# Kernel tuning notes

Measured on AMD Instinct MI355X. Metric: run time of the kernel, lower is better.

## Reference

```python
import jax, jax.numpy as jnp
import numpy as np

EPS = 2.0 ** (-20)  # FP16_tiny
Q_DIM = 256
M_DIM = 256
NUM_HEAD = 8
KEY_DIM = Q_DIM // NUM_HEAD   # 32 per head
VAL_DIM = M_DIM // NUM_HEAD   # 32 per head
OUT_DIM = 256
B, R, S = 1, 256, 1024


def setup_inputs() -> dict:
    key = jax.random.key(0)
    ks = jax.random.split(key, 12)
    q_data = jax.random.normal(ks[0], (B, R, S, Q_DIM), dtype=jnp.float32)
    m_data = jax.random.normal(ks[1], (B, R, S, M_DIM), dtype=jnp.float32)
    q_mask = (jax.random.uniform(ks[2], (B, R, S, 1)) > 0.1).astype(jnp.float32)
    bias = jax.random.normal(ks[3], (B, R, 1, S), dtype=jnp.float32) * 0.1
    # weights stored as [in, out] (torch Linear applies x @ W.T; equivalent math)
    gl = lambda k, i, o: jax.random.normal(k, (i, o), dtype=jnp.float32) * (6.0 / (i + o)) ** 0.5
    Wq = gl(ks[4], Q_DIM, NUM_HEAD * KEY_DIM)
    Wk = gl(ks[5], M_DIM, KEY_DIM)
    Wv = gl(ks[6], M_DIM, VAL_DIM)
    # linear_o has 'final' init (zeros) in the original; use small random for a useful baseline
    Wo = jax.random.normal(ks[7], (NUM_HEAD * VAL_DIM, OUT_DIM), dtype=jnp.float32) * 0.02
    bo = jnp.zeros((OUT_DIM,), dtype=jnp.float32)
    # linear_g: 'gating' init is W=0, b=1; use small random W for non-degenerate test
    Wg = jax.random.normal(ks[8], (Q_DIM, NUM_HEAD * VAL_DIM), dtype=jnp.float32) * 0.02
    bg = jnp.ones((NUM_HEAD * VAL_DIM,), dtype=jnp.float32)
    return {"q_data": q_data, "m_data": m_data, "q_mask": q_mask, "bias": bias,
            "Wq": Wq, "Wk": Wk, "Wv": Wv, "Wo": Wo, "bo": bo, "Wg": Wg, "bg": bg}


def reference(q_data, m_data, q_mask, bias, Wq, Wk, Wv, Wo, bo, Wg, bg):
    key_scalar = KEY_DIM ** (-0.5)
    # masked mean pool over the sequence (N_seq) axis -> [B,R,q_dim]
    q_avg = jnp.sum(q_data * q_mask, axis=-2) / (jnp.sum(q_mask, axis=-2) + EPS)
    q = (q_avg @ Wq) * key_scalar                       # [B,R,H*kd]
    q = q.reshape(q.shape[:-1] + (NUM_HEAD, KEY_DIM))    # [B,R,H,kd]
    k = m_data @ Wk                                      # [B,R,S,kd]
    v = m_data @ Wv                                      # [B,R,S,vd]
    logits = jnp.einsum('brhd,brsd->brhs', q, k) + bias  # [B,R,H,S]
    weight = jax.nn.softmax(logits, axis=-1)
    weighted_avg = jnp.einsum('brhs,brsd->brhd', weight, v)  # [B,R,H,vd]
    # gating
    g = jax.nn.sigmoid(q_data @ Wg + bg)                 # [B,R,S,H*vd]
    g = g.reshape(g.shape[:-1] + (NUM_HEAD, VAL_DIM))     # [B,R,S,H,vd]
    gated = weighted_avg[:, :, None] * g                  # [B,R,S,H,vd]
    gated = gated.reshape(gated.shape[:-2] + (NUM_HEAD * VAL_DIM,))
    out = gated @ Wo + bo                                 # [B,R,S,out_dim]
    return out
```

## Files before the change

kernel.cpp:

```cpp
#include <hip/hip_runtime.h>
#include <stdint.h>

typedef __bf16 bf16x8 __attribute__((ext_vector_type(8)));
typedef float f32x4 __attribute__((ext_vector_type(4)));
typedef unsigned short ushort8 __attribute__((ext_vector_type(8)));
typedef unsigned short u16x4 __attribute__((ext_vector_type(4)));

#define S_DIM 1024
#define R_DIM 256
#define DMODEL 256
#define EPSV 9.5367431640625e-07f
#define ASTRIDE 264
#define OSTRIDE 72

__device__ __forceinline__ unsigned short f2bf(float f) {
  uint32_t u = __float_as_uint(f);
  u += 0x7fffu + ((u >> 16) & 1u);
  return (unsigned short)(u >> 16);
}
__device__ __forceinline__ float bf2f(unsigned short s) {
  return __uint_as_float(((uint32_t)s) << 16);
}
__device__ __forceinline__ bf16x8 ldfrag(const unsigned short* p) {
  return __builtin_bit_cast(bf16x8, *(const ushort8*)p);
}
__device__ __forceinline__ bf16x8 pack8(float4 a, float4 b) {
  ushort8 u;
  u[0] = f2bf(a.x); u[1] = f2bf(a.y); u[2] = f2bf(a.z); u[3] = f2bf(a.w);
  u[4] = f2bf(b.x); u[5] = f2bf(b.y); u[6] = f2bf(b.z); u[7] = f2bf(b.w);
  return __builtin_bit_cast(bf16x8, u);
}

__global__ __launch_bounds__(256) void pack_all_kernel(const float* __restrict__ Wk,
                                                       const float* __restrict__ Wv,
                                                       const float* __restrict__ Wg,
                                                       const float* __restrict__ Wo,
                                                       unsigned short* __restrict__ wkv,
                                                       unsigned short* __restrict__ wg_p,
                                                       unsigned short* __restrict__ wo_p) {
  int bid = blockIdx.x;
  int tid = threadIdx.x;
  if (bid < 64) {
    int idx = bid * 256 + tid;
    int j = idx & 7, lane = (idx >> 3) & 63, t = idx >> 9;
    int ct = t & 3, kstep = t >> 2;
    int k = kstep * 32 + ((lane >> 4) << 3) + j;
    int col = ct * 16 + (lane & 15);
    float w = (col < 32) ? Wk[k * 32 + col] : Wv[k * 32 + (col - 32)];
    wkv[idx] = f2bf(w);
  } else {
    const float* W = (bid < 320) ? Wg : Wo;
    unsigned short* out = (bid < 320) ? wg_p : wo_p;
    int idx = ((bid < 320) ? (bid - 64) : (bid - 320)) * 256 + tid;
    int j = idx & 7, lane = (idx >> 3) & 63, t = idx >> 9;
    int ct = t & 15, kstep = t >> 4;
    int k = kstep * 32 + ((lane >> 4) << 3) + j;
    int col = ct * 16 + (lane & 15);
    out[idx] = f2bf(W[k * 256 + col]);
  }
}

template <int USE_ECHO>
__global__ __launch_bounds__(512, 4) void pool_kernel(const float* __restrict__ q_data,
                                                      const float* __restrict__ q_mask,
                                                      float* __restrict__ psum,
                                                      float* __restrict__ pmask,
                                                      unsigned short* __restrict__ qb16) {
  __shared__ float mlds[256];
  __shared__ float wred[4];
  __shared__ f32x4 red[8 * 64];
  int bid = blockIdx.x;
  int tid = threadIdx.x;
  int r = bid >> 2, c = bid & 3;
  int s0 = c * 256;
  if (tid < 256) {
    float m = q_mask[r * S_DIM + s0 + tid];
    mlds[tid] = m;
    float ms = m;
    for (int off = 32; off; off >>= 1) ms += __shfl_down(ms, off);
    if ((tid & 63) == 0) wred[tid >> 6] = ms;
  }
  __syncthreads();
  if (tid == 0) pmask[r * 4 + c] = wred[0] + wred[1] + wred[2] + wred[3];
  int wv = tid >> 6, ln = tid & 63;
  size_t rowbase = (size_t)(r * S_DIM + s0);
  const float* bp = q_data + (rowbase + wv) * DMODEL + ln * 4;
  unsigned short* ebp = USE_ECHO ? (qb16 + (rowbase + wv) * DMODEL + ln * 4) : nullptr;
  f32x4 acc4 = {};
  #pragma unroll 8
  for (int it = 0; it < 32; it++) {
    float4 v = *(const float4*)(bp + (size_t)it * 8 * DMODEL);
    float mm = mlds[it * 8 + wv];
    acc4[0] += v.x * mm; acc4[1] += v.y * mm;
    acc4[2] += v.z * mm; acc4[3] += v.w * mm;
    if (USE_ECHO) {
      u16x4 e;
      e[0] = f2bf(v.x); e[1] = f2bf(v.y); e[2] = f2bf(v.z); e[3] = f2bf(v.w);
      *(u16x4*)(ebp + (size_t)it * 8 * DMODEL) = e;
    }
  }
  red[wv * 64 + ln] = acc4;
  __syncthreads();
  if (tid < 256) {
    int c4 = tid >> 2, cm = tid & 3;
    float sum = 0.f;
    #pragma unroll
    for (int k = 0; k < 8; k++) sum += red[k * 64 + c4][cm];
    psum[(r * 4 + c) * 256 + tid] = sum;
  }
}

__global__ __launch_bounds__(256, 8) void kv_kernel(const float* __restrict__ m_data,
                                                    const unsigned short* __restrict__ wkv,
                                                    unsigned short* __restrict__ kb,
                                                    unsigned short* __restrict__ vb_t) {
  __shared__ __align__(16) unsigned short As[32 * ASTRIDE];
  int bid = blockIdx.x;
  int tid = threadIdx.x;
  int wave = tid >> 6, lane = tid & 63;
  int g = lane >> 4, lr = lane & 15;
  int row0 = bid * 32;
  #pragma unroll
  for (int i = 0; i < 4; i++) {
    int c = i * 256 + tid;
    int ra = c >> 5, cc = c & 31;
    const float4* p = (const float4*)&m_data[(size_t)(row0 + ra) * DMODEL + cc * 8];
    *(ushort8*)&As[ra * ASTRIDE + cc * 8] = __builtin_bit_cast(ushort8, pack8(p[0], p[1]));
  }
  __syncthreads();
  int rt = wave >> 1, cp = (wave & 1) * 2;
  f32x4 acc[2] = {};
  #pragma unroll
  for (int ks = 0; ks < 8; ks++) {
    bf16x8 af = ldfrag(&As[(rt * 16 + lr) * ASTRIDE + ks * 32 + g * 8]);
    #pragma unroll
    for (int cc2 = 0; cc2 < 2; cc2++) {
      bf16x8 bf = ldfrag(&wkv[((ks * 4 + cp + cc2) << 9) + lane * 8]);
      acc[cc2] = __builtin_amdgcn_mfma_f32_16x16x32_bf16(af, bf, acc[cc2], 0, 0, 0);
    }
  }
  __syncthreads();
  unsigned short* O = As;
  #pragma unroll
  for (int cc2 = 0; cc2 < 2; cc2++) {
    #pragma unroll
    for (int rg = 0; rg < 4; rg++) {
      O[(rt * 16 + g * 4 + rg) * OSTRIDE + (cp + cc2) * 16 + lr] = f2bf(acc[cc2][rg]);
    }
  }
  __syncthreads();
  {
    int rowl = tid >> 3, c4 = (tid & 7) * 4;
    u16x4 v = *(const u16x4*)&O[rowl * OSTRIDE + c4];
    *(u16x4*)&kb[(size_t)(row0 + rowl) * 32 + c4] = v;
  }
  if (tid < 128) {
    int d = tid >> 2, s8 = (tid & 3) * 8;
    ushort8 v;
    #pragma unroll
    for (int j = 0; j < 8; j++) v[j] = O[(s8 + j) * OSTRIDE + 32 + d];
    int ra = row0 >> 10, sl0 = row0 & 1023;
    *(ushort8*)&vb_t[((size_t)(ra * 32) + d) * S_DIM + sl0 + s8] = v;
  }
}

__global__ __launch_bounds__(256) void attn2_kernel(const unsigned short* __restrict__ kb,
                                                    const unsigned short* __restrict__ vb_t,
                                                    const float* __restrict__ psum,
                                                    const float* __restrict__ pmask,
                                                    const float* __restrict__ Wq,
                                                    const float* __restrict__ bias,
                                                    float* __restrict__ wavg) {
  int r = blockIdx.x, tid = threadIdx.x;
  int w = tid >> 6, lane = tid & 63, g = lane >> 4, lr = lane & 15;
  __shared__ float qa[256];
  __shared__ float qsp[8 * 33];
  __shared__ float lgp[8 * 1028];
  __shared__ float paccL[8 * 64 * 4];
  __shared__ float denom[8];
  float s4 = psum[(r * 4 + 0) * 256 + tid] + psum[(r * 4 + 1) * 256 + tid] +
             psum[(r * 4 + 2) * 256 + tid] + psum[(r * 4 + 3) * 256 + tid];
  float msum = pmask[r * 4] + pmask[r * 4 + 1] + pmask[r * 4 + 2] + pmask[r * 4 + 3];
  qa[tid] = s4 / (msum + EPSV);
  __syncthreads();
  float qacc = 0.f;
  #pragma unroll 8
  for (int d = 0; d < 256; d++) qacc += qa[d] * Wq[d * 256 + tid];
  qsp[(tid >> 5) * 33 + (tid & 31)] = qacc * 0.17677669529663687f;
  __syncthreads();
  ushort8 uq;
  #pragma unroll
  for (int j = 0; j < 8; j++)
    uq[j] = (lr < 8) ? f2bf(qsp[lr * 33 + g * 8 + j]) : (unsigned short)0;
  bf16x8 qf = __builtin_bit_cast(bf16x8, uq);
  for (int i = 0; i < 16; i++) {
    int rt = w * 16 + i;
    bf16x8 af = ldfrag(&kb[((size_t)r * S_DIM + rt * 16 + lr) * 32 + g * 8]);
    f32x4 d4 = {};
    d4 = __builtin_amdgcn_mfma_f32_16x16x32_bf16(af, qf, d4, 0, 0, 0);
    if (lr < 8) {
      #pragma unroll
      for (int rg = 0; rg < 4; rg++) {
        int sv = rt * 16 + g * 4 + rg;
        lgp[lr * 1028 + sv] = d4[rg] + bias[r * S_DIM + sv];
      }
    }
  }
  __syncthreads();
  for (int hh = 0; hh < 2; hh++) {
    int h = w * 2 + hh;
    float mx = -1e30f;
    #pragma unroll
    for (int i = 0; i < 16; i++) mx = fmaxf(mx, lgp[h * 1028 + lane + i * 64]);
    for (int off = 32; off; off >>= 1) mx = fmaxf(mx, __shfl_xor(mx, off));
    float sum = 0.f;
    #pragma unroll
    for (int i = 0; i < 16; i++) {
      float e = __expf(lgp[h * 1028 + lane + i * 64] - mx);
      lgp[h * 1028 + lane + i * 64] = e;
      sum += e;
    }
    for (int off = 32; off; off >>= 1) sum += __shfl_xor(sum, off);
    if (lane == 0) denom[h] = sum;
  }
  __syncthreads();
  f32x4 pv[2] = {};
  for (int kk = 0; kk < 8; kk++) {
    int ks = w * 8 + kk;
    bf16x8 pa;
    if (lr < 8) {
      const float4* pp = (const float4*)&lgp[lr * 1028 + ks * 32 + g * 8];
      pa = pack8(*(const float4*)&pp[0], *(const float4*)&pp[1]);
    } else {
      pa = __builtin_bit_cast(bf16x8, (ushort8)(unsigned short)0);
    }
    #pragma unroll
    for (int ct = 0; ct < 2; ct++) {
      bf16x8 vf = ldfrag(&vb_t[((size_t)(r * 32) + ct * 16 + lr) * S_DIM + ks * 32 + g * 8]);
      pv[ct] = __builtin_amdgcn_mfma_f32_16x16x32_bf16(pa, vf, pv[ct], 0, 0, 0);
    }
  }
  *(f32x4*)&paccL[((w * 2 + 0) * 64 + lane) * 4] = pv[0];
  *(f32x4*)&paccL[((w * 2 + 1) * 64 + lane) * 4] = pv[1];
  __syncthreads();
  {
    int h = tid >> 5, d = tid & 31;
    int ct = d >> 4, l2 = (h >> 2) * 16 + (d & 15), rg = h & 3;
    float sum = 0.f;
    #pragma unroll
    for (int w4 = 0; w4 < 4; w4++) sum += paccL[((w4 * 2 + ct) * 64 + l2) * 4 + rg];
    wavg[r * 256 + tid] = __fdividef(sum, denom[h]);
  }
}

template <int USE_BF16>
__global__ __launch_bounds__(512, 4) void gate3_kernel(const float* __restrict__ q_data,
                                                       const unsigned short* __restrict__ qb16,
                                                       const unsigned short* __restrict__ wg,
                                                       const unsigned short* __restrict__ wo,
                                                       const float* __restrict__ bgv,
                                                       const float* __restrict__ bov,
                                                       const float* __restrict__ wavg,
                                                       float* __restrict__ outp) {
  __shared__ unsigned short AsG[64 * ASTRIDE];
  __shared__ float wavs[256];
  __shared__ float bgs[256];
  __shared__ float bos[256];
  int bid = blockIdx.x;
  int r = bid >> 4, sc = bid & 15;
  int tid = threadIdx.x;
  int wave = tid >> 6, lane = tid & 63, g = lane >> 4, lr = lane & 15;
  int row0g = r * S_DIM + sc * 64;
  if (tid < 256) {
    wavs[tid] = wavg[r * 256 + tid];
    bgs[tid] = bgv[tid];
    bos[tid] = bov[tid];
  }
  #pragma unroll
  for (int i = 0; i < 4; i++) {
    int c = i * 512 + tid;
    int ra = c >> 5, cc = c & 31;
    ushort8 v;
    if (USE_BF16) {
      v = *(const ushort8*)&qb16[(size_t)(row0g + ra) * DMODEL + cc * 8];
    } else {
      const float4* p = (const float4*)&q_data[(size_t)(row0g + ra) * DMODEL + cc * 8];
      v = __builtin_bit_cast(ushort8, pack8(p[0], p[1]));
    }
    *(ushort8*)&AsG[ra * ASTRIDE + cc * 8] = v;
  }
  __syncthreads();
  f32x4 acc[4][2] = {};
  for (int ks = 0; ks < 8; ks++) {
    bf16x8 b0 = ldfrag(&wg[((ks * 16 + 2 * wave) << 9) + lane * 8]);
    bf16x8 b1 = ldfrag(&wg[((ks * 16 + 2 * wave + 1) << 9) + lane * 8]);
    bf16x8 af[4];
    #pragma unroll
    for (int rt = 0; rt < 4; rt++)
      af[rt] = ldfrag(&AsG[(rt * 16 + lr) * ASTRIDE + ks * 32 + g * 8]);
    #pragma unroll
    for (int rt = 0; rt < 4; rt++) {
      acc[rt][0] = __builtin_amdgcn_mfma_f32_16x16x32_bf16(af[rt], b0, acc[rt][0], 0, 0, 0);
      acc[rt][1] = __builtin_amdgcn_mfma_f32_16x16x32_bf16(af[rt], b1, acc[rt][1], 0, 0, 0);
    }
  }
  __syncthreads();
  #pragma unroll
  for (int rt = 0; rt < 4; rt++) {
    #pragma unroll
    for (int c0 = 0; c0 < 2; c0++) {
      int col = (wave * 2 + c0) * 16 + lr;
      float wv = wavs[col];
      float bgc = bgs[col];
      #pragma unroll
      for (int rg = 0; rg < 4; rg++) {
        int row = rt * 16 + g * 4 + rg;
        float x = acc[rt][c0][rg] + bgc;
        float sg = __fdividef(1.0f, 1.0f + __expf(-x));
        AsG[row * ASTRIDE + col] = f2bf(sg * wv);
      }
    }
  }
  __syncthreads();
  f32x4 acc2[4][2] = {};
  for (int ks = 0; ks < 8; ks++) {
    bf16x8 b0 = ldfrag(&wo[((ks * 16 + 2 * wave) << 9) + lane * 8]);
    bf16x8 b1 = ldfrag(&wo[((ks * 16 + 2 * wave + 1) << 9) + lane * 8]);
    bf16x8 af[4];
    #pragma unroll
    for (int rt = 0; rt < 4; rt++)
      af[rt] = ldfrag(&AsG[(rt * 16 + lr) * ASTRIDE + ks * 32 + g * 8]);
    #pragma unroll
    for (int rt = 0; rt < 4; rt++) {
      acc2[rt][0] = __builtin_amdgcn_mfma_f32_16x16x32_bf16(af[rt], b0, acc2[rt][0], 0, 0, 0);
      acc2[rt][1] = __builtin_amdgcn_mfma_f32_16x16x32_bf16(af[rt], b1, acc2[rt][1], 0, 0, 0);
    }
  }
  #pragma unroll
  for (int rt = 0; rt < 4; rt++) {
    #pragma unroll
    for (int c0 = 0; c0 < 2; c0++) {
      int col = (wave * 2 + c0) * 16 + lr;
      float boc = bos[col];
      #pragma unroll
      for (int rg = 0; rg < 4; rg++) {
        int row = rt * 16 + g * 4 + rg;
        outp[(size_t)(row0g + row) * DMODEL + col] = acc2[rt][c0][rg] + boc;
      }
    }
  }
}

extern "C" void kernel_launch(void* const* d_in, const int* in_sizes, int n_in,
                              void* d_out, int out_size, void* d_ws, size_t ws_size,
                              hipStream_t stream) {
  const float* q_data = (const float*)d_in[0];
  const float* m_data = (const float*)d_in[1];
  const float* q_mask = (const float*)d_in[2];
  const float* bias   = (const float*)d_in[3];
  const float* Wq     = (const float*)d_in[4];
  const float* Wk     = (const float*)d_in[5];
  const float* Wv     = (const float*)d_in[6];
  const float* Wo     = (const float*)d_in[7];
  const float* bo     = (const float*)d_in[8];
  const float* Wg     = (const float*)d_in[9];
  const float* bg     = (const float*)d_in[10];
  float* outp = (float*)d_out;

  char* ws = (char*)d_ws;
  unsigned short* kb      = (unsigned short*)(ws + 0);
  unsigned short* vb_t    = (unsigned short*)(ws + 16777216);
  unsigned short* wkv     = (unsigned short*)(ws + 33554432);
  unsigned short* wg_pack = (unsigned short*)(ws + 33587200);
  unsigned short* wo_pack = (unsigned short*)(ws + 33718272);
  float* psum  = (float*)(ws + 33849344);
  float* pmask = (float*)(ws + 34897920);
  float* wavg  = (float*)(ws + 35164160);
  const size_t QB16_OFF = 35651584;
  const size_t QB16_BYTES = (size_t)R_DIM * S_DIM * DMODEL * 2;
  bool use_echo = ws_size >= QB16_OFF + QB16_BYTES;
  unsigned short* qb16 = use_echo ? (unsigned short*)(ws + QB16_OFF) : nullptr;

  pack_all_kernel<<<576, 256, 0, stream>>>(Wk, Wv, Wg, Wo, wkv, wg_pack, wo_pack);
  kv_kernel<<<8192, 256, 0, stream>>>(m_data, wkv, kb, vb_t);
  if (use_echo)
    pool_kernel<1><<<1024, 512, 0, stream>>>(q_data, q_mask, psum, pmask, qb16);
  else
    pool_kernel<0><<<1024, 512, 0, stream>>>(q_data, q_mask, psum, pmask, nullptr);
  attn2_kernel<<<256, 256, 0, stream>>>(kb, vb_t, psum, pmask, Wq, bias, wavg);
  if (use_echo)
    gate3_kernel<1><<<4096, 512, 0, stream>>>(q_data, qb16, wg_pack, wo_pack, bg, bo, wavg, outp);
  else
    gate3_kernel<0><<<4096, 512, 0, stream>>>(q_data, nullptr, wg_pack, wo_pack, bg, bo, wavg, outp);
}
```

Baseline: 304.6 us.

## Use direct global-to-LDS loads in kv kernel and XCD-aware block remapping

The kv projection kernel now stages fp32 m_data rows straight into LDS through global_load_lds with an XOR swizzle. Conversion to bf16 moves to the fragment read, and the tile shrinks to 16 rows per block, which doubles the grid. The pool, kv and gate kernels also remap block IDs so consecutive work lands on the same XCD, aiming for better L2 locality across the chiplets. The trade-offs are twice the LDS footprint per row (fp32 instead of bf16), more blocks, and conversion work repeated inside the MFMA loop.

```diff
diff --git a/kernel.cpp b/kernel.cpp
--- a/kernel.cpp
+++ b/kernel.cpp
@@ -69,7 +69,8 @@
   __shared__ float mlds[256];
   __shared__ float wred[4];
   __shared__ f32x4 red[8 * 64];
-  int bid = blockIdx.x;
+  int bid0 = blockIdx.x;
+  int bid = (bid0 & 7) * 128 + (bid0 >> 3);
   int tid = threadIdx.x;
   int r = bid >> 2, c = bid & 3;
   int s0 = c * 256;
@@ -114,48 +115,45 @@
                                                     const unsigned short* __restrict__ wkv,
                                                     unsigned short* __restrict__ kb,
                                                     unsigned short* __restrict__ vb_t) {
-  __shared__ __align__(16) unsigned short As[32 * ASTRIDE];
-  int bid = blockIdx.x;
+  __shared__ __align__(16) float Af[16 * 256];
+  int bid0 = blockIdx.x;
+  int bid = (bid0 & 7) * 2048 + (bid0 >> 3);
   int tid = threadIdx.x;
   int wave = tid >> 6, lane = tid & 63;
   int g = lane >> 4, lr = lane & 15;
-  int row0 = bid * 32;
+  int row0 = bid * 16;
   #pragma unroll
   for (int i = 0; i < 4; i++) {
-    int c = i * 256 + tid;
-    int ra = c >> 5, cc = c & 31;
-    const float4* p = (const float4*)&m_data[(size_t)(row0 + ra) * DMODEL + cc * 8];
-    *(ushort8*)&As[ra * ASTRIDE + cc * 8] = __builtin_bit_cast(ushort8, pack8(p[0], p[1]));
-  }
-  __syncthreads();
-  int rt = wave >> 1, cp = (wave & 1) * 2;
-  f32x4 acc[2] = {};
+    int C = wave * 4 + i;
+    const char* gsrc = (const char*)(m_data + (size_t)(row0 + C) * DMODEL)
+                     + ((lane * 16) ^ ((C & 7) << 5));
+    __builtin_amdgcn_global_load_lds(
+        (const __attribute__((address_space(1))) void*)gsrc,
+        (__attribute__((address_space(3))) void*)(&Af[C * 256]), 16, 0, 0);
+  }
+  __syncthreads();
+  f32x4 acc = {};
   #pragma unroll
   for (int ks = 0; ks < 8; ks++) {
-    bf16x8 af = ldfrag(&As[(rt * 16 + lr) * ASTRIDE + ks * 32 + g * 8]);
-    #pragma unroll
-    for (int cc2 = 0; cc2 < 2; cc2++) {
-      bf16x8 bf = ldfrag(&wkv[((ks * 4 + cp + cc2) << 9) + lane * 8]);
-      acc[cc2] = __builtin_amdgcn_mfma_f32_16x16x32_bf16(af, bf, acc[cc2], 0, 0, 0);
-    }
-  }
-  __syncthreads();
-  unsigned short* O = As;
-  #pragma unroll
-  for (int cc2 = 0; cc2 < 2; cc2++) {
-    #pragma unroll
-    for (int rg = 0; rg < 4; rg++) {
-      O[(rt * 16 + g * 4 + rg) * OSTRIDE + (cp + cc2) * 16 + lr] = f2bf(acc[cc2][rg]);
-    }
-  }
-  __syncthreads();
-  {
+    int boff = (ks * 128 + g * 32) ^ ((lr & 7) << 5);
+    const float4* fp = (const float4*)((const char*)Af + lr * 1024 + boff);
+    bf16x8 af = pack8(fp[0], fp[1]);
+    bf16x8 bf = ldfrag(&wkv[((ks * 4 + wave) << 9) + lane * 8]);
+    acc = __builtin_amdgcn_mfma_f32_16x16x32_bf16(af, bf, acc, 0, 0, 0);
+  }
+  __syncthreads();
+  unsigned short* O = (unsigned short*)Af;
+  #pragma unroll
+  for (int rg = 0; rg < 4; rg++)
+    O[(g * 4 + rg) * OSTRIDE + wave * 16 + lr] = f2bf(acc[rg]);
+  __syncthreads();
+  if (tid < 128) {
     int rowl = tid >> 3, c4 = (tid & 7) * 4;
     u16x4 v = *(const u16x4*)&O[rowl * OSTRIDE + c4];
     *(u16x4*)&kb[(size_t)(row0 + rowl) * 32 + c4] = v;
-  }
-  if (tid < 128) {
-    int d = tid >> 2, s8 = (tid & 3) * 8;
+  } else if (tid < 192) {
+    int t = tid - 128;
+    int d = t >> 1, s8 = (t & 1) * 8;
     ushort8 v;
     #pragma unroll
     for (int j = 0; j < 8; j++) v[j] = O[(s8 + j) * OSTRIDE + 32 + d];
@@ -266,7 +264,8 @@
   __shared__ float wavs[256];
   __shared__ float bgs[256];
   __shared__ float bos[256];
-  int bid = blockIdx.x;
+  int bid0 = blockIdx.x;
+  int bid = (bid0 & 7) * 512 + (bid0 >> 3);
   int r = bid >> 4, sc = bid & 15;
   int tid = threadIdx.x;
   int wave = tid >> 6, lane = tid & 63, g = lane >> 4, lr = lane & 15;
@@ -382,7 +381,7 @@
   unsigned short* qb16 = use_echo ? (unsigned short*)(ws + QB16_OFF) : nullptr;
 
   pack_all_kernel<<<576, 256, 0, stream>>>(Wk, Wv, Wg, Wo, wkv, wg_pack, wo_pack);
-  kv_kernel<<<8192, 256, 0, stream>>>(m_data, wkv, kb, vb_t);
+  kv_kernel<<<16384, 256, 0, stream>>>(m_data, wkv, kb, vb_t);
   if (use_echo)
     pool_kernel<1><<<1024, 512, 0, stream>>>(q_data, q_mask, psum, pmask, qb16);
   else
```

Measured after the change: 309.7 us. No clear change (+1.7%).

## Fuse pooling with gate GEMM and sigmoid, store bf16 gate for output kernel

Applied to the files above, without the earlier changes.

Merges masked mean pooling with the gating GEMM and sigmoid in one kernel, so q_data is read once and the bf16 sigmoid gate is written to workspace. The final kernel reads that gate, scales it by the attention weighted average and runs only the output GEMM. This removes the bf16 echo of q_data and the second gating GEMM from the stage that runs after attention. In exchange, partial pooling sums are finer-grained (16 per row instead of 4), attention reduces more partials, and the gate is rounded to bf16 before being multiplied by the weighted average.

```diff
diff --git a/kernel.cpp b/kernel.cpp
--- a/kernel.cpp
+++ b/kernel.cpp
@@ -60,56 +60,6 @@
   }
 }
 
-template <int USE_ECHO>
-__global__ __launch_bounds__(512, 4) void pool_kernel(const float* __restrict__ q_data,
-                                                      const float* __restrict__ q_mask,
-                                                      float* __restrict__ psum,
-                                                      float* __restrict__ pmask,
-                                                      unsigned short* __restrict__ qb16) {
-  __shared__ float mlds[256];
-  __shared__ float wred[4];
-  __shared__ f32x4 red[8 * 64];
-  int bid = blockIdx.x;
-  int tid = threadIdx.x;
-  int r = bid >> 2, c = bid & 3;
-  int s0 = c * 256;
-  if (tid < 256) {
-    float m = q_mask[r * S_DIM + s0 + tid];
-    mlds[tid] = m;
-    float ms = m;
-    for (int off = 32; off; off >>= 1) ms += __shfl_down(ms, off);
-    if ((tid & 63) == 0) wred[tid >> 6] = ms;
-  }
-  __syncthreads();
-  if (tid == 0) pmask[r * 4 + c] = wred[0] + wred[1] + wred[2] + wred[3];
-  int wv = tid >> 6, ln = tid & 63;
-  size_t rowbase = (size_t)(r * S_DIM + s0);
-  const float* bp = q_data + (rowbase + wv) * DMODEL + ln * 4;
-  unsigned short* ebp = USE_ECHO ? (qb16 + (rowbase + wv) * DMODEL + ln * 4) : nullptr;
-  f32x4 acc4 = {};
-  #pragma unroll 8
-  for (int it = 0; it < 32; it++) {
-    float4 v = *(const float4*)(bp + (size_t)it * 8 * DMODEL);
-    float mm = mlds[it * 8 + wv];
-    acc4[0] += v.x * mm; acc4[1] += v.y * mm;
-    acc4[2] += v.z * mm; acc4[3] += v.w * mm;
-    if (USE_ECHO) {
-      u16x4 e;
-      e[0] = f2bf(v.x); e[1] = f2bf(v.y); e[2] = f2bf(v.z); e[3] = f2bf(v.w);
-      *(u16x4*)(ebp + (size_t)it * 8 * DMODEL) = e;
-    }
-  }
-  red[wv * 64 + ln] = acc4;
-  __syncthreads();
-  if (tid < 256) {
-    int c4 = tid >> 2, cm = tid & 3;
-    float sum = 0.f;
-    #pragma unroll
-    for (int k = 0; k < 8; k++) sum += red[k * 64 + c4][cm];
-    psum[(r * 4 + c) * 256 + tid] = sum;
-  }
-}
-
 __global__ __launch_bounds__(256, 8) void kv_kernel(const float* __restrict__ m_data,
                                                     const unsigned short* __restrict__ wkv,
                                                     unsigned short* __restrict__ kb,
@@ -161,6 +111,92 @@
     for (int j = 0; j < 8; j++) v[j] = O[(s8 + j) * OSTRIDE + 32 + d];
     int ra = row0 >> 10, sl0 = row0 & 1023;
     *(ushort8*)&vb_t[((size_t)(ra * 32) + d) * S_DIM + sl0 + s8] = v;
+  }
+}
+
+template <int WRITE_G>
+__global__ __launch_bounds__(512) void poolgate_kernel(const float* __restrict__ q_data,
+                                                       const float* __restrict__ q_mask,
+                                                       const unsigned short* __restrict__ wg,
+                                                       const float* __restrict__ bgv,
+                                                       float* __restrict__ psum,
+                                                       float* __restrict__ pmask,
+                                                       unsigned short* __restrict__ Gout) {
+  __shared__ unsigned short AsG[64 * ASTRIDE];
+  __shared__ float mlds[64];
+  __shared__ f32x4 red[8 * 64];
+  __shared__ float bgs[256];
+  int bid = blockIdx.x;
+  int r = bid >> 4, sc = bid & 15;
+  int tid = threadIdx.x;
+  int wave = tid >> 6, lane = tid & 63, g = lane >> 4, lr = lane & 15;
+  int row0g = r * S_DIM + sc * 64;
+  if (tid < 64) mlds[tid] = q_mask[row0g + tid];
+  if (tid >= 256) bgs[tid - 256] = bgv[tid - 256];
+  __syncthreads();
+  if (tid < 64) {
+    float ms = mlds[tid];
+    for (int off = 32; off; off >>= 1) ms += __shfl_down(ms, off);
+    if (tid == 0) pmask[r * 16 + sc] = ms;
+  }
+  f32x4 acc4 = {};
+  int cc = tid & 63;
+  #pragma unroll
+  for (int i = 0; i < 8; i++) {
+    int ra = i * 8 + wave;
+    float4 v = *(const float4*)&q_data[(size_t)(row0g + ra) * DMODEL + cc * 4];
+    float mm = mlds[ra];
+    acc4[0] += v.x * mm; acc4[1] += v.y * mm;
+    acc4[2] += v.z * mm; acc4[3] += v.w * mm;
+    u16x4 e;
+    e[0] = f2bf(v.x); e[1] = f2bf(v.y); e[2] = f2bf(v.z); e[3] = f2bf(v.w);
+    *(u16x4*)&AsG[ra * ASTRIDE + cc * 4] = e;
+  }
+  red[wave * 64 + cc] = acc4;
+  __syncthreads();
+  if (tid < 256) {
+    float sum = 0.f;
+    #pragma unroll
+    for (int k = 0; k < 8; k++) sum += red[k * 64 + (tid >> 2)][tid & 3];
+    psum[((size_t)(r * 16 + sc)) * 256 + tid] = sum;
+  }
+  if (WRITE_G) {
+    f32x4 acc[4][2] = {};
+    for (int ks = 0; ks < 8; ks++) {
+      bf16x8 b0 = ldfrag(&wg[((ks * 16 + 2 * wave) << 9) + lane * 8]);
+      bf16x8 b1 = ldfrag(&wg[((ks * 16 + 2 * wave + 1) << 9) + lane * 8]);
+      bf16x8 af[4];
+      #pragma unroll
+      for (int rt = 0; rt < 4; rt++)
+        af[rt] = ldfrag(&AsG[(rt * 16 + lr) * ASTRIDE + ks * 32 + g * 8]);
+      #pragma unroll
+      for (int rt = 0; rt < 4; rt++) {
+        acc[rt][0] = __builtin_amdgcn_mfma_f32_16x16x32_bf16(af[rt], b0, acc[rt][0], 0, 0, 0);
+        acc[rt][1] = __builtin_amdgcn_mfma_f32_16x16x32_bf16(af[rt], b1, acc[rt][1], 0, 0, 0);
+      }
+    }
+    __syncthreads();
+    #pragma unroll
+    for (int rt = 0; rt < 4; rt++) {
+      #pragma unroll
+      for (int c0 = 0; c0 < 2; c0++) {
+        int col = (wave * 2 + c0) * 16 + lr;
+        float bgc = bgs[col];
+        #pragma unroll
+        for (int rg = 0; rg < 4; rg++) {
+          int row = rt * 16 + g * 4 + rg;
+          float x = acc[rt][c0][rg] + bgc;
+          AsG[row * ASTRIDE + col] = f2bf(__fdividef(1.0f, 1.0f + __expf(-x)));
+        }
+      }
+    }
+    __syncthreads();
+    #pragma unroll
+    for (int i = 0; i < 4; i++) {
+      int c = i * 512 + tid;
+      int ra = c >> 5, c8 = (c & 31) * 8;
+      *(ushort8*)&Gout[(size_t)(row0g + ra) * DMODEL + c8] = *(const ushort8*)&AsG[ra * ASTRIDE + c8];
+    }
   }
 }
 
@@ -178,9 +214,12 @@
   __shared__ float lgp[8 * 1028];
   __shared__ float paccL[8 * 64 * 4];
   __shared__ float denom[8];
-  float s4 = psum[(r * 4 + 0) * 256 + tid] + psum[(r * 4 + 1) * 256 + tid] +
-             psum[(r * 4 + 2) * 256 + tid] + psum[(r * 4 + 3) * 256 + tid];
-  float msum = pmask[r * 4] + pmask[r * 4 + 1] + pmask[r * 4 + 2] + pmask[r * 4 + 3];
+  float s4 = 0.f;
+  #pragma unroll
+  for (int p = 0; p < 16; p++) s4 += psum[((size_t)(r * 16 + p)) * 256 + tid];
+  float msum = 0.f;
+  #pragma unroll
+  for (int p = 0; p < 16; p++) msum += pmask[r * 16 + p];
   qa[tid] = s4 / (msum + EPSV);
   __syncthreads();
   float qacc = 0.f;
@@ -253,9 +292,63 @@
   }
 }
 
-template <int USE_BF16>
+__global__ __launch_bounds__(512) void gate4_kernel(const unsigned short* __restrict__ G,
+                                                    const unsigned short* __restrict__ wo,
+                                                    const float* __restrict__ bov,
+                                                    const float* __restrict__ wavg,
+                                                    float* __restrict__ outp) {
+  __shared__ unsigned short AsG[64 * ASTRIDE];
+  __shared__ float wavs[256];
+  __shared__ float bos[256];
+  int bid = blockIdx.x;
+  int r = bid >> 4, sc = bid & 15;
+  int tid = threadIdx.x;
+  int wave = tid >> 6, lane = tid & 63, g = lane >> 4, lr = lane & 15;
+  int row0g = r * S_DIM + sc * 64;
+  if (tid < 256) wavs[tid] = wavg[r * 256 + tid];
+  else           bos[tid - 256] = bov[tid - 256];
+  __syncthreads();
+  #pragma unroll
+  for (int i = 0; i < 4; i++) {
+    int c = i * 512 + tid;
+    int ra = c >> 5, c8 = (c & 31) * 8;
+    ushort8 gv = *(const ushort8*)&G[(size_t)(row0g + ra) * DMODEL + c8];
+    ushort8 o;
+    #pragma unroll
+    for (int j = 0; j < 8; j++) o[j] = f2bf(bf2f(gv[j]) * wavs[c8 + j]);
+    *(ushort8*)&AsG[ra * ASTRIDE + c8] = o;
+  }
+  __syncthreads();
+  f32x4 acc2[4][2] = {};
+  for (int ks = 0; ks < 8; ks++) {
+    bf16x8 b0 = ldfrag(&wo[((ks * 16 + 2 * wave) << 9) + lane * 8]);
+    bf16x8 b1 = ldfrag(&wo[((ks * 16 + 2 * wave + 1) << 9) + lane * 8]);
+    bf16x8 af[4];
+    #pragma unroll
+    for (int rt = 0; rt < 4; rt++)
+      af[rt] = ldfrag(&AsG[(rt * 16 + lr) * ASTRIDE + ks * 32 + g * 8]);
+    #pragma unroll
+    for (int rt = 0; rt < 4; rt++) {
+      acc2[rt][0] = __builtin_amdgcn_mfma_f32_16x16x32_bf16(af[rt], b0, acc2[rt][0], 0, 0, 0);
+      acc2[rt][1] = __builtin_amdgcn_mfma_f32_16x16x32_bf16(af[rt], b1, acc2[rt][1], 0, 0, 0);
+    }
+  }
+  #pragma unroll
+  for (int rt = 0; rt < 4; rt++) {
+    #pragma unroll
+    for (int c0 = 0; c0 < 2; c0++) {
+      int col = (wave * 2 + c0) * 16 + lr;
+      float boc = bos[col];
+      #pragma unroll
+      for (int rg = 0; rg < 4; rg++) {
+        int row = rt * 16 + g * 4 + rg;
+        outp[(size_t)(row0g + row) * DMODEL + col] = acc2[rt][c0][rg] + boc;
+      }
+    }
+  }
+}
+
 __global__ __launch_bounds__(512, 4) void gate3_kernel(const float* __restrict__ q_data,
-                                                       const unsigned short* __restrict__ qb16,
                                                        const unsigned short* __restrict__ wg,
                                                        const unsigned short* __restrict__ wo,
                                                        const float* __restrict__ bgv,
@@ -280,14 +373,8 @@
   for (int i = 0; i < 4; i++) {
     int c = i * 512 + tid;
     int ra = c >> 5, cc = c & 31;
-    ushort8 v;
-    if (USE_BF16) {
-      v = *(const ushort8*)&qb16[(size_t)(row0g + ra) * DMODEL + cc * 8];
-    } else {
-      const float4* p = (const float4*)&q_data[(size_t)(row0g + ra) * DMODEL + cc * 8];
-      v = __builtin_bit_cast(ushort8, pack8(p[0], p[1]));
-    }
-    *(ushort8*)&AsG[ra * ASTRIDE + cc * 8] = v;
+    const float4* p = (const float4*)&q_data[(size_t)(row0g + ra) * DMODEL + cc * 8];
+    *(ushort8*)&AsG[ra * ASTRIDE + cc * 8] = __builtin_bit_cast(ushort8, pack8(p[0], p[1]));
   }
   __syncthreads();
   f32x4 acc[4][2] = {};
@@ -374,22 +461,22 @@
   unsigned short* wg_pack = (unsigned short*)(ws + 33587200);
   unsigned short* wo_pack = (unsigned short*)(ws + 33718272);
   float* psum  = (float*)(ws + 33849344);
-  float* pmask = (float*)(ws + 34897920);
-  float* wavg  = (float*)(ws + 35164160);
-  const size_t QB16_OFF = 35651584;
-  const size_t QB16_BYTES = (size_t)R_DIM * S_DIM * DMODEL * 2;
-  bool use_echo = ws_size >= QB16_OFF + QB16_BYTES;
-  unsigned short* qb16 = use_echo ? (unsigned short*)(ws + QB16_OFF) : nullptr;
+  float* pmask = (float*)(ws + 38043648);
+  float* wavg  = (float*)(ws + 38060032);
+  const size_t G_OFF = 38322176;
+  const size_t G_BYTES = (size_t)R_DIM * S_DIM * DMODEL * 2;
+  bool use_g = ws_size >= G_OFF + G_BYTES;
+  unsigned short* Gbuf = use_g ? (unsigned short*)(ws + G_OFF) : nullptr;
 
   pack_all_kernel<<<576, 256, 0, stream>>>(Wk, Wv, Wg, Wo, wkv, wg_pack, wo_pack);
   kv_kernel<<<8192, 256, 0, stream>>>(m_data, wkv, kb, vb_t);
-  if (use_echo)
-    pool_kernel<1><<<1024, 512, 0, stream>>>(q_data, q_mask, psum, pmask, qb16);
+  if (use_g)
+    poolgate_kernel<1><<<4096, 512, 0, stream>>>(q_data, q_mask, wg_pack, bg, psum, pmask, Gbuf);
   else
-    pool_kernel<0><<<1024, 512, 0, stream>>>(q_data, q_mask, psum, pmask, nullptr);
+    poolgate_kernel<0><<<4096, 512, 0, stream>>>(q_data, q_mask, wg_pack, bg, psum, pmask, nullptr);
   attn2_kernel<<<256, 256, 0, stream>>>(kb, vb_t, psum, pmask, Wq, bias, wavg);
-  if (use_echo)
-    gate3_kernel<1><<<4096, 512, 0, stream>>>(q_data, qb16, wg_pack, wo_pack, bg, bo, wavg, outp);
+  if (use_g)
+    gate4_kernel<<<4096, 512, 0, stream>>>(Gbuf, wo_pack, bo, wavg, outp);
   else
-    gate3_kernel<0><<<4096, 512, 0, stream>>>(q_data, nullptr, wg_pack, wo_pack, bg, bo, wavg, outp);
-}
+    gate3_kernel<<<4096, 512, 0, stream>>>(q_data, wg_pack, wo_pack, bg, bo, wavg, outp);
+}
```

After: 306.2 us. About the same (+0.5%).
